# Kernel tuning notes

Hardware: AMD Instinct MI355X
Metric: run time of the kernel (lower is better)

The kernel has to match this reference:

```python
import jax, jax.numpy as jnp
import numpy as np
from jax import lax

B, T, C, DIN, DOUT = 32, 128, 64, 32, 32  # batch, output_channels(seq), input_channels, input_dim, output_dim


def _init_params(key):
    # Mirror torch init: xOps zeros with identity on min(dout,din) diag; hOps = eye.
    # Add small noise so gradients/behavior are non-degenerate.
    k1, k2 = jax.random.split(key)
    eye_x = jnp.zeros((DOUT, DIN), jnp.float32).at[jnp.arange(min(DOUT, DIN)), jnp.arange(min(DOUT, DIN))].set(1.0)
    xOps = jnp.broadcast_to(eye_x, (4, T, C, DOUT, DIN)) + 0.02 * jax.random.normal(k1, (4, T, C, DOUT, DIN), jnp.float32)
    hOps = jnp.broadcast_to(jnp.eye(DOUT, dtype=jnp.float32), (4, T, C, DOUT, DOUT)) + 0.02 * jax.random.normal(k2, (4, T, C, DOUT, DOUT), jnp.float32)
    return xOps, hOps


def setup_inputs() -> dict:
    key = jax.random.key(0)
    kx, kp = jax.random.split(key)
    x = jax.random.normal(kx, (B, T, C, DIN), jnp.float32)
    xOps, hOps = _init_params(kp)
    return {"x": x, "xOps": xOps, "hOps": hOps}


def reference(x, xOps, hOps):
    # x: [B,T,C,Din]; xOps: [4,T,C,Dout,Din]; hOps: [4,T,C,Dout,Dout]
    b, t, c, _ = x.shape
    dout = hOps.shape[-1]
    h0 = jnp.zeros((b, c, dout), x.dtype)
    c0 = jnp.zeros((b, c, dout), x.dtype)

    def step(carry, inp):
        h, cc = carry
        x_t, xop_t, hop_t = inp  # [B,C,Din], [4,C,Dout,Din], [4,C,Dout,Dout]
        # per-channel (grouped) gate pre-activations, 4 gates at once
        X = jnp.einsum('gcij,bcj->gbci', xop_t, x_t) + jnp.einsum('gcij,bcj->gbci', hop_t, h)
        i = jax.nn.sigmoid(X[0])
        f = jax.nn.sigmoid(X[1])
        g = jnp.tanh(X[2])
        o = jax.nn.sigmoid(X[3])
        c_new = f * cc + i * g
        h_new = o * jnp.tanh(c_new)
        return (h_new, c_new), None

    xs = (jnp.swapaxes(x, 0, 1), jnp.swapaxes(xOps, 0, 1), jnp.swapaxes(hOps, 0, 1))
    (h_fin, _), _ = lax.scan(step, (h0, c0), xs)
    return h_fin  # [B,C,Dout]
```

## Files before the change

### kernel.cpp

```cpp
#include <hip/hip_runtime.h>
#include <stdint.h>

#define T_STEPS 128
#define C_CH    64
#define HS      40

using frag_ab = __attribute__((ext_vector_type(8))) short;
using frag_cd = __attribute__((ext_vector_type(4))) float;
typedef __attribute__((ext_vector_type(4))) uint32_t u32x4;

__device__ __forceinline__ uint32_t pack_hi16(uint32_t u0, uint32_t u1) {
  return __builtin_amdgcn_perm(u1, u0, 0x07060302u);
}

__device__ __forceinline__ float fast_sigmoid(float v) {
  return __builtin_amdgcn_rcpf(1.0f + __expf(-v));
}
__device__ __forceinline__ float fast_tanh(float v) {
  return fmaf(2.0f, __builtin_amdgcn_rcpf(1.0f + __expf(-2.0f * v)), -1.0f);
}

struct Frag2 { frag_ab hi, lo; };

__device__ __forceinline__ Frag2 split8(float4 a, float4 b) {
  uint32_t u0 = __float_as_uint(a.x), u1 = __float_as_uint(a.y);
  uint32_t u2 = __float_as_uint(a.z), u3 = __float_as_uint(a.w);
  uint32_t u4 = __float_as_uint(b.x), u5 = __float_as_uint(b.y);
  uint32_t u6 = __float_as_uint(b.z), u7 = __float_as_uint(b.w);
  uint32_t r0 = __float_as_uint(a.x - __uint_as_float(u0 & 0xFFFF0000u));
  uint32_t r1 = __float_as_uint(a.y - __uint_as_float(u1 & 0xFFFF0000u));
  uint32_t r2 = __float_as_uint(a.z - __uint_as_float(u2 & 0xFFFF0000u));
  uint32_t r3 = __float_as_uint(a.w - __uint_as_float(u3 & 0xFFFF0000u));
  uint32_t r4 = __float_as_uint(b.x - __uint_as_float(u4 & 0xFFFF0000u));
  uint32_t r5 = __float_as_uint(b.y - __uint_as_float(u5 & 0xFFFF0000u));
  uint32_t r6 = __float_as_uint(b.z - __uint_as_float(u6 & 0xFFFF0000u));
  uint32_t r7 = __float_as_uint(b.w - __uint_as_float(u7 & 0xFFFF0000u));
  union { u32x4 v; frag_ab f; } H, L;
  H.v[0] = pack_hi16(u0, u1); H.v[1] = pack_hi16(u2, u3);
  H.v[2] = pack_hi16(u4, u5); H.v[3] = pack_hi16(u6, u7);
  L.v[0] = pack_hi16(r0, r1); L.v[1] = pack_hi16(r2, r3);
  L.v[2] = pack_hi16(r4, r5); L.v[3] = pack_hi16(r6, r7);
  Frag2 o; o.hi = H.f; o.lo = L.f; return o;
}

__global__ void __launch_bounds__(512, 2)
lstm_kernel(const float* __restrict__ x, const float* __restrict__ xOps,
            const float* __restrict__ hOps, float* __restrict__ out) {
  __shared__ short Hhi[2][16][HS];
  __shared__ short Hlo[2][16][HS];

  const int tid    = threadIdx.x;
  const int c      = blockIdx.x & 63;
  const int q      = blockIdx.x >> 6;
  const int w      = tid >> 6;
  const int lane   = tid & 63;
  const int frag_n = lane & 15;
  const int quad   = lane >> 4;

  const int g  = frag_n & 3;
  const int iw = 4 * w + (frag_n >> 2);
  const size_t woff = ((size_t)g * T_STEPS * C_CH + c) * 1024
                    + (size_t)iw * 32 + quad * 8;
  const int bcl = (q * 8 + frag_n) & 31;
  const size_t xoff = ((size_t)bcl * T_STEPS * C_CH + c) * 32 + quad * 8;

  for (int idx = tid; idx < 2 * 16 * HS; idx += 512) {
    ((short*)Hhi)[idx] = 0; ((short*)Hlo)[idx] = 0;
  }
  __syncthreads();

  float4 wv[4][6];
#pragma unroll
  for (int s = 0; s < 3; ++s) {
    const float* pw = xOps + (size_t)s * (C_CH * 1024) + woff;
    wv[s][0] = ((const float4*)pw)[0];
    wv[s][1] = ((const float4*)pw)[1];
    const float* ph = hOps + (size_t)s * (C_CH * 1024) + woff;
    wv[s][2] = ((const float4*)ph)[0];
    wv[s][3] = ((const float4*)ph)[1];
    const float* px = x + (size_t)s * (C_CH * 32) + xoff;
    wv[s][4] = ((const float4*)px)[0];
    wv[s][5] = ((const float4*)px)[1];
  }

  const int hrd = quad * 8;
  const int iq  = 4 * w + quad;
  float c_state = 0.0f;

  for (int tb = 0; tb < T_STEPS; tb += 4) {
#pragma unroll
    for (int u = 0; u < 4; ++u) {
      const int t  = tb + u;
      const int cs = u;
      const int ps = (u + 3) & 3;

      Frag2 A0 = split8(wv[cs][0], wv[cs][1]);
      Frag2 A1 = split8(wv[cs][2], wv[cs][3]);
      Frag2 BX = split8(wv[cs][4], wv[cs][5]);
      frag_cd ax = {0.f, 0.f, 0.f, 0.f};
      ax = __builtin_amdgcn_mfma_f32_16x16x32_bf16(A0.hi, BX.hi, ax, 0, 0, 0);
      ax = __builtin_amdgcn_mfma_f32_16x16x32_bf16(A0.hi, BX.lo, ax, 0, 0, 0);
      ax = __builtin_amdgcn_mfma_f32_16x16x32_bf16(A0.lo, BX.hi, ax, 0, 0, 0);

      if (t + 3 < T_STEPS) {
        const float* pw = xOps + (size_t)(t + 3) * (C_CH * 1024) + woff;
        wv[ps][0] = ((const float4*)pw)[0];
        wv[ps][1] = ((const float4*)pw)[1];
        const float* ph = hOps + (size_t)(t + 3) * (C_CH * 1024) + woff;
        wv[ps][2] = ((const float4*)ph)[0];
        wv[ps][3] = ((const float4*)ph)[1];
        const float* px = x + (size_t)(t + 3) * (C_CH * 32) + xoff;
        wv[ps][4] = ((const float4*)px)[0];
        wv[ps][5] = ((const float4*)px)[1];
      }

      asm volatile("s_waitcnt lgkmcnt(0)\n\ts_barrier" ::: "memory");

      const int p = t & 1;
      const frag_ab bh = *(const frag_ab*)&Hhi[p][frag_n][hrd];
      const frag_ab bl = *(const frag_ab*)&Hlo[p][frag_n][hrd];
      frag_cd ah = {0.f, 0.f, 0.f, 0.f};
      ah = __builtin_amdgcn_mfma_f32_16x16x32_bf16(A1.hi, bh, ah, 0, 0, 0);
      ah = __builtin_amdgcn_mfma_f32_16x16x32_bf16(A1.hi, bl, ah, 0, 0, 0);
      ah = __builtin_amdgcn_mfma_f32_16x16x32_bf16(A1.lo, bh, ah, 0, 0, 0);

      const float ig = fast_sigmoid(ax[0] + ah[0]);
      const float fg = fast_sigmoid(ax[1] + ah[1]);
      const float gg = fast_tanh(ax[2] + ah[2]);
      const float og = fast_sigmoid(ax[3] + ah[3]);
      c_state = fg * c_state + ig * gg;
      const float hval = og * fast_tanh(c_state);

      if (t == T_STEPS - 1) {
        if (frag_n < 8)
          out[((size_t)(q * 8 + frag_n) * C_CH + c) * 32 + iq] = hval;
      } else if (frag_n < 8) {
        const uint32_t uh = __float_as_uint(hval);
        const float    rh = hval - __uint_as_float(uh & 0xFFFF0000u);
        Hhi[p ^ 1][frag_n][iq] = (short)(uh >> 16);
        Hlo[p ^ 1][frag_n][iq] = (short)(__float_as_uint(rh) >> 16);
      }
    }
  }
}

extern "C" void kernel_launch(void* const* d_in, const int* in_sizes, int n_in,
                              void* d_out, int out_size, void* d_ws, size_t ws_size,
                              hipStream_t stream) {
  const float* x    = (const float*)d_in[0];
  const float* xOps = (const float*)d_in[1];
  const float* hOps = (const float*)d_in[2];
  lstm_kernel<<<dim3(256), dim3(512), 0, stream>>>(x, xOps, hOps, (float*)d_out);
}
```

Baseline: 375.4 us.

## Split batch across more blocks, stage x via async LDS loads, shorten prefetch

Each block now handles 4 batch rows instead of 8, so the grid doubles to 512 blocks and launch bounds allow 4 blocks per CU. This spreads the serial recurrence across more CUs. The x tile is loaded by one wave straight into double-buffered shared memory with global_load_lds, using an XOR swizzle, instead of every lane loading it into registers. The weight prefetch depth drops from 3 steps to 1 step, and each step now waits on vmcnt(0) at the barrier. This lowers register pressure, but global load latency is exposed on each of the 128 serial steps.

```diff
diff --git a/kernel.cpp b/kernel.cpp
--- a/kernel.cpp
+++ b/kernel.cpp
@@ -18,6 +18,11 @@
 }
 __device__ __forceinline__ float fast_tanh(float v) {
   return fmaf(2.0f, __builtin_amdgcn_rcpf(1.0f + __expf(-2.0f * v)), -1.0f);
+}
+
+__device__ __forceinline__ void async_load16(const float* g, void* l) {
+  __builtin_amdgcn_global_load_lds((const __attribute__((address_space(1))) void*)g,
+                                   (__attribute__((address_space(3))) void*)l, 16, 0, 0);
 }
 
 struct Frag2 { frag_ab hi, lo; };
@@ -43,15 +48,16 @@
   Frag2 o; o.hi = H.f; o.lo = L.f; return o;
 }
 
-__global__ void __launch_bounds__(512, 2)
+__global__ void __launch_bounds__(512, 4)
 lstm_kernel(const float* __restrict__ x, const float* __restrict__ xOps,
             const float* __restrict__ hOps, float* __restrict__ out) {
-  __shared__ short Hhi[2][16][HS];
-  __shared__ short Hlo[2][16][HS];
+  __shared__ __align__(16) float Bx[2][16][32];
+  __shared__ __align__(16) short Hhi[2][16][HS];
+  __shared__ __align__(16) short Hlo[2][16][HS];
 
   const int tid    = threadIdx.x;
   const int c      = blockIdx.x & 63;
-  const int q      = blockIdx.x >> 6;
+  const int qq     = blockIdx.x >> 6;
   const int w      = tid >> 6;
   const int lane   = tid & 63;
   const int frag_n = lane & 15;
@@ -61,87 +67,80 @@
   const int iw = 4 * w + (frag_n >> 2);
   const size_t woff = ((size_t)g * T_STEPS * C_CH + c) * 1024
                     + (size_t)iw * 32 + quad * 8;
-  const int bcl = (q * 8 + frag_n) & 31;
-  const size_t xoff = ((size_t)bcl * T_STEPS * C_CH + c) * 32 + quad * 8;
+  const float* pwx = xOps + woff;
+  const float* pwh = hOps + woff;
 
-  for (int idx = tid; idx < 2 * 16 * HS; idx += 512) {
-    ((short*)Hhi)[idx] = 0; ((short*)Hlo)[idx] = 0;
+  const int xrow = lane >> 3;
+  const float* xsrc = x + ((size_t)(qq * 4 + (xrow & 3)) * T_STEPS * C_CH + c) * 32
+                        + (((lane & 7) ^ (xrow & 7)) << 2);
+
+  for (int idx = tid; idx < 2 * 16 * 32; idx += 512) ((float*)Bx)[idx] = 0.f;
+  for (int idx = tid; idx < 2 * 16 * HS / 2; idx += 512) {
+    ((uint32_t*)Hhi)[idx] = 0u; ((uint32_t*)Hlo)[idx] = 0u;
   }
-  __syncthreads();
+  asm volatile("s_waitcnt lgkmcnt(0)\n\ts_barrier" ::: "memory");
 
-  float4 wv[4][6];
-#pragma unroll
-  for (int s = 0; s < 3; ++s) {
-    const float* pw = xOps + (size_t)s * (C_CH * 1024) + woff;
-    wv[s][0] = ((const float4*)pw)[0];
-    wv[s][1] = ((const float4*)pw)[1];
-    const float* ph = hOps + (size_t)s * (C_CH * 1024) + woff;
-    wv[s][2] = ((const float4*)ph)[0];
-    wv[s][3] = ((const float4*)ph)[1];
-    const float* px = x + (size_t)s * (C_CH * 32) + xoff;
-    wv[s][4] = ((const float4*)px)[0];
-    wv[s][5] = ((const float4*)px)[1];
-  }
+  float4 wvA[4], wvB[4];
+  wvA[0] = ((const float4*)pwx)[0]; wvA[1] = ((const float4*)pwx)[1];
+  wvA[2] = ((const float4*)pwh)[0]; wvA[3] = ((const float4*)pwh)[1];
+  if (w == 7) async_load16(xsrc, &Bx[0][0][0]);
 
+  const int bs0 = (((quad << 1) ^ (frag_n & 7)) << 2);
+  const int bs1 = ((((quad << 1) | 1) ^ (frag_n & 7)) << 2);
   const int hrd = quad * 8;
   const int iq  = 4 * w + quad;
   float c_state = 0.0f;
 
-  for (int tb = 0; tb < T_STEPS; tb += 4) {
-#pragma unroll
-    for (int u = 0; u < 4; ++u) {
-      const int t  = tb + u;
-      const int cs = u;
-      const int ps = (u + 3) & 3;
+#define STEP(T, CUR, NXT, PAR)                                                  \
+  do {                                                                          \
+            \
+    asm volatile("s_waitcnt vmcnt(0) lgkmcnt(0)\n\ts_barrier" ::: "memory");    \
+    if ((T) + 1 < T_STEPS) {    \
+      pwx += C_CH * 1024;                                                       \
+      NXT[0] = ((const float4*)pwx)[0]; NXT[1] = ((const float4*)pwx)[1];       \
+      pwh += C_CH * 1024;                                                       \
+      NXT[2] = ((const float4*)pwh)[0]; NXT[3] = ((const float4*)pwh)[1];       \
+      if (w == 7) {                                                             \
+        xsrc += C_CH * 32;                                                      \
+        async_load16(xsrc, &Bx[(PAR) ^ 1][0][0]);                               \
+      }                                                                         \
+    }                                                                           \
+    Frag2 A0 = split8(CUR[0], CUR[1]);                           \
+    Frag2 A1 = split8(CUR[2], CUR[3]);                           \
+    const float* Bp = &Bx[PAR][frag_n][0];                                      \
+    Frag2 BX = split8(*(const float4*)(Bp + bs0), *(const float4*)(Bp + bs1));  \
+    frag_cd ax = {0.f, 0.f, 0.f, 0.f};                                          \
+    ax = __builtin_amdgcn_mfma_f32_16x16x32_bf16(A0.hi, BX.hi, ax, 0, 0, 0);    \
+    ax = __builtin_amdgcn_mfma_f32_16x16x32_bf16(A0.hi, BX.lo, ax, 0, 0, 0);    \
+    ax = __builtin_amdgcn_mfma_f32_16x16x32_bf16(A0.lo, BX.hi, ax, 0, 0, 0);    \
+    const frag_ab bh = *(const frag_ab*)&Hhi[PAR][frag_n][hrd];                 \
+    const frag_ab bl = *(const frag_ab*)&Hlo[PAR][frag_n][hrd];                 \
+    frag_cd ah = {0.f, 0.f, 0.f, 0.f};                                          \
+    ah = __builtin_amdgcn_mfma_f32_16x16x32_bf16(A1.hi, bh, ah, 0, 0, 0);       \
+    ah = __builtin_amdgcn_mfma_f32_16x16x32_bf16(A1.hi, bl, ah, 0, 0, 0);       \
+    ah = __builtin_amdgcn_mfma_f32_16x16x32_bf16(A1.lo, bh, ah, 0, 0, 0);       \
+    const float ig = fast_sigmoid(ax[0] + ah[0]);                               \
+    const float fg = fast_sigmoid(ax[1] + ah[1]);                               \
+    const float gg = fast_tanh(ax[2] + ah[2]);                                  \
+    const float og = fast_sigmoid(ax[3] + ah[3]);                               \
+    c_state = fg * c_state + ig * gg;                                           \
+    const float hval = og * fast_tanh(c_state);                                 \
+    if ((T) == T_STEPS - 1) {                                                   \
+      if (frag_n < 4)                                                           \
+        out[((size_t)(qq * 4 + frag_n) * C_CH + c) * 32 + iq] = hval;           \
+    } else if (frag_n < 4) {                                                    \
+      const uint32_t uh = __float_as_uint(hval);                                \
+      const float    rh = hval - __uint_as_float(uh & 0xFFFF0000u);             \
+      Hhi[(PAR) ^ 1][frag_n][iq] = (short)(uh >> 16);                           \
+      Hlo[(PAR) ^ 1][frag_n][iq] = (short)(__float_as_uint(rh) >> 16);          \
+    }                                                                           \
+  } while (0)
 
-      Frag2 A0 = split8(wv[cs][0], wv[cs][1]);
-      Frag2 A1 = split8(wv[cs][2], wv[cs][3]);
-      Frag2 BX = split8(wv[cs][4], wv[cs][5]);
-      frag_cd ax = {0.f, 0.f, 0.f, 0.f};
-      ax = __builtin_amdgcn_mfma_f32_16x16x32_bf16(A0.hi, BX.hi, ax, 0, 0, 0);
-      ax = __builtin_amdgcn_mfma_f32_16x16x32_bf16(A0.hi, BX.lo, ax, 0, 0, 0);
-      ax = __builtin_amdgcn_mfma_f32_16x16x32_bf16(A0.lo, BX.hi, ax, 0, 0, 0);
-
-      if (t + 3 < T_STEPS) {
-        const float* pw = xOps + (size_t)(t + 3) * (C_CH * 1024) + woff;
-        wv[ps][0] = ((const float4*)pw)[0];
-        wv[ps][1] = ((const float4*)pw)[1];
-        const float* ph = hOps + (size_t)(t + 3) * (C_CH * 1024) + woff;
-        wv[ps][2] = ((const float4*)ph)[0];
-        wv[ps][3] = ((const float4*)ph)[1];
-        const float* px = x + (size_t)(t + 3) * (C_CH * 32) + xoff;
-        wv[ps][4] = ((const float4*)px)[0];
-        wv[ps][5] = ((const float4*)px)[1];
-      }
-
-      asm volatile("s_waitcnt lgkmcnt(0)\n\ts_barrier" ::: "memory");
-
-      const int p = t & 1;
-      const frag_ab bh = *(const frag_ab*)&Hhi[p][frag_n][hrd];
-      const frag_ab bl = *(const frag_ab*)&Hlo[p][frag_n][hrd];
-      frag_cd ah = {0.f, 0.f, 0.f, 0.f};
-      ah = __builtin_amdgcn_mfma_f32_16x16x32_bf16(A1.hi, bh, ah, 0, 0, 0);
-      ah = __builtin_amdgcn_mfma_f32_16x16x32_bf16(A1.hi, bl, ah, 0, 0, 0);
-      ah = __builtin_amdgcn_mfma_f32_16x16x32_bf16(A1.lo, bh, ah, 0, 0, 0);
-
-      const float ig = fast_sigmoid(ax[0] + ah[0]);
-      const float fg = fast_sigmoid(ax[1] + ah[1]);
-      const float gg = fast_tanh(ax[2] + ah[2]);
-      const float og = fast_sigmoid(ax[3] + ah[3]);
-      c_state = fg * c_state + ig * gg;
-      const float hval = og * fast_tanh(c_state);
-
-      if (t == T_STEPS - 1) {
-        if (frag_n < 8)
-          out[((size_t)(q * 8 + frag_n) * C_CH + c) * 32 + iq] = hval;
-      } else if (frag_n < 8) {
-        const uint32_t uh = __float_as_uint(hval);
-        const float    rh = hval - __uint_as_float(uh & 0xFFFF0000u);
-        Hhi[p ^ 1][frag_n][iq] = (short)(uh >> 16);
-        Hlo[p ^ 1][frag_n][iq] = (short)(__float_as_uint(rh) >> 16);
-      }
-    }
+  for (int tb = 0; tb < T_STEPS; tb += 2) {
+    STEP(tb,     wvA, wvB, 0);
+    STEP(tb + 1, wvB, wvA, 1);
   }
+#undef STEP
 }
 
 extern "C" void kernel_launch(void* const* d_in, const int* in_sizes, int n_in,
@@ -150,5 +149,5 @@
   const float* x    = (const float*)d_in[0];
   const float* xOps = (const float*)d_in[1];
   const float* hOps = (const float*)d_in[2];
-  lstm_kernel<<<dim3(256), dim3(512), 0, stream>>>(x, xOps, hOps, (float*)d_out);
+  lstm_kernel<<<dim3(512), dim3(512), 0, stream>>>(x, xOps, hOps, (float*)d_out);
 }
```

Result: slower. 453.0 us (+20.7%).
